# Optimization experiments

Measured on AMD Instinct MI355X. Metric: run time of the kernel, lower is better.

Reference implementation:

```python
import jax, jax.numpy as jnp
import numpy as np

DIM = 768
D_STATE = 16
D_CONV = 4
EXPAND = 2
VOCAB = 50257
N_LAYERS = 4
D_INNER = EXPAND * DIM
B, S = 1, 1024
EPS = 1e-6


def setup_inputs() -> dict:
    key = jax.random.key(0)
    ks = jax.random.split(key, 8)
    s = 0.02
    L = N_LAYERS
    tokens = jax.random.randint(ks[0], (B, S), 0, VOCAB, dtype=jnp.int32)
    embedding = jax.random.normal(ks[1], (VOCAB, DIM), dtype=jnp.float32) * s
    norm_w = jnp.ones((L, DIM), dtype=jnp.float32)
    in_proj_w = jax.random.normal(ks[2], (L, 2 * D_INNER, DIM), dtype=jnp.float32) * s
    conv_w = jax.random.normal(ks[3], (L, D_INNER, 1, D_CONV), dtype=jnp.float32) * s
    conv_b = jnp.zeros((L, D_INNER), dtype=jnp.float32)
    x_proj_w = jax.random.normal(ks[4], (L, D_INNER + 2 * D_STATE, D_INNER), dtype=jnp.float32) * s
    dt_w = jax.random.normal(ks[5], (L, D_INNER, D_INNER), dtype=jnp.float32) * s
    dt_b = jnp.zeros((L, D_INNER), dtype=jnp.float32)
    A_log = jnp.broadcast_to(jnp.log(jnp.arange(1, D_STATE + 1, dtype=jnp.float32)), (L, D_INNER, D_STATE)) + jnp.zeros((L, D_INNER, D_STATE), dtype=jnp.float32)
    D = jnp.ones((L, D_INNER), dtype=jnp.float32)
    out_proj_w = jax.random.normal(ks[6], (L, DIM, D_INNER), dtype=jnp.float32) * s
    normf_w = jnp.ones((DIM,), dtype=jnp.float32)
    lm_head_w = jax.random.normal(ks[7], (VOCAB, DIM), dtype=jnp.float32) * s
    return {"tokens": tokens, "embedding": embedding, "norm_w": norm_w,
            "in_proj_w": in_proj_w, "conv_w": conv_w, "conv_b": conv_b,
            "x_proj_w": x_proj_w, "dt_w": dt_w, "dt_b": dt_b,
            "A_log": A_log, "D": D, "out_proj_w": out_proj_w,
            "normf_w": normf_w, "lm_head_w": lm_head_w}


def _rmsnorm(x, w):
    v = jnp.mean(jnp.square(x.astype(jnp.float32)), axis=-1, keepdims=True)
    return w * (x * jax.lax.rsqrt(v + EPS)).astype(w.dtype)


def _ssm(x, x_proj_w, dt_w, dt_b, A_log, D):
    # x: [B,S,Di]
    xp = jnp.einsum('bsd,ed->bse', x, x_proj_w)  # [B,S,Di+2N]
    dt_in = xp[..., :D_INNER]
    Bm = xp[..., D_INNER:D_INNER + D_STATE]      # [B,S,N]
    Cm = xp[..., D_INNER + D_STATE:]             # [B,S,N]
    dt = jax.nn.softplus(jnp.einsum('bsd,ed->bse', dt_in, dt_w) + dt_b)  # [B,S,Di]
    A = -jnp.exp(A_log)                          # [Di,N]
    dA = jnp.exp(dt[..., None] * A)              # [B,S,Di,N]
    dBx = (dt * x)[..., None] * Bm[:, :, None, :]  # [B,S,Di,N]

    def step(h, inp):
        dA_t, dBx_t, C_t = inp
        h = h * dA_t + dBx_t                     # [B,Di,N]
        y_t = jnp.einsum('bdn,bn->bd', h, C_t)   # [B,Di]
        return h, y_t

    h0 = jnp.zeros((x.shape[0], D_INNER, D_STATE), dtype=x.dtype)
    _, ys = jax.lax.scan(step, h0, (dA.swapaxes(0, 1), dBx.swapaxes(0, 1), Cm.swapaxes(0, 1)))
    return ys.swapaxes(0, 1) + D * x


def _block(x, p):
    nw, ipw, cw, cb, xpw, dtw, dtb, alog, d, opw = p
    res = x
    x = _rmsnorm(x, nw)
    xz = jnp.einsum('bsd,ed->bse', x, ipw)       # [B,S,2*Di]
    xc, z = jnp.split(xz, 2, axis=-1)
    # causal depthwise conv (pad left by d_conv-1, truncate to seq_len)
    xt = xc.transpose(0, 2, 1)                   # [B,Di,S]
    xt = jax.lax.conv_general_dilated(xt, cw, (1,), [(D_CONV - 1, 0)],
                                      dimension_numbers=('NCH', 'OIH', 'NCH'),
                                      feature_group_count=D_INNER)
    xc = xt.transpose(0, 2, 1) + cb
    xc = jax.nn.silu(xc)
    y = _ssm(xc, xpw, dtw, dtb, alog, d)
    out = jnp.einsum('bsd,ed->bse', y * jax.nn.silu(z), opw)
    return res + out


def reference(tokens, embedding, norm_w, in_proj_w, conv_w, conv_b, x_proj_w,
              dt_w, dt_b, A_log, D, out_proj_w, normf_w, lm_head_w):
    x = embedding[tokens]                        # [B,S,DIM]
    params = (norm_w, in_proj_w, conv_w, conv_b, x_proj_w, dt_w, dt_b, A_log, D, out_proj_w)
    x, _ = jax.lax.scan(lambda c, p: (_block(c, p), None), x, params)
    x = _rmsnorm(x, normf_w)
    return jnp.einsum('bsd,vd->bsv', x, lm_head_w)  # logits [B,S,VOCAB]
```

## Files before the change

kernel.cpp:

```cpp
#include <hip/hip_runtime.h>
#include <cstddef>
#include <cstdint>

#define DIM 768
#define DINNER 1536
#define DSTATE 16
#define NLAYERS 4
#define SEQ 1024
#define XPROJ_N 1568
#define VOCAB 50257
#define NCHUNK 128
#define CHL 8

typedef float f32x4 __attribute__((ext_vector_type(4)));
typedef __bf16 bf16x8 __attribute__((ext_vector_type(8)));
typedef __bf16 bf16x4 __attribute__((ext_vector_type(4)));

typedef __attribute__((address_space(1))) const unsigned int as1_u32;
typedef __attribute__((address_space(3))) unsigned int as3_u32;

__device__ __forceinline__ void gl_lds16(const void* g, void* l) {
  __builtin_amdgcn_global_load_lds((as1_u32*)g, (as3_u32*)l, 16, 0, 0);
}

__device__ __forceinline__ float siluf_(float x) {
  return x / (1.f + __expf(-x));
}
__device__ __forceinline__ float softplusf_(float x) {
  return (x > 20.f) ? x : log1pf(expf(x));
}

__global__ __launch_bounds__(256) void k_cvt(const float* __restrict__ src,
                                             __bf16* __restrict__ dst, int n) {
  int e = (blockIdx.x * 256 + threadIdx.x) << 2;
  if (e >= n) return;
  f32x4 v = *(const f32x4*)(src + e);
  bf16x4 h;
  h.x = (__bf16)v.x; h.y = (__bf16)v.y; h.z = (__bf16)v.z; h.w = (__bf16)v.w;
  *(bf16x4*)(dst + e) = h;
}

__global__ __launch_bounds__(256) void k_embed(const int* __restrict__ tok,
                                               const float* __restrict__ emb,
                                               float* __restrict__ X) {
  int i4 = blockIdx.x * 256 + threadIdx.x;
  int s = i4 / 192;
  int d4 = i4 - s * 192;
  const f32x4* src = (const f32x4*)(emb + (size_t)tok[s] * DIM);
  ((f32x4*)X)[i4] = src[d4];
}

__global__ __launch_bounds__(256) void k_rmsnorm(const float* __restrict__ x,
                                                 const float* __restrict__ w,
                                                 __bf16* __restrict__ o) {
  int s = blockIdx.x;
  const float* xr = x + (size_t)s * DIM;
  __bf16* orow = o + (size_t)s * DIM;
  int t = threadIdx.x;
  float v0 = xr[t], v1 = xr[t + 256], v2 = xr[t + 512];
  float acc = v0 * v0 + v1 * v1 + v2 * v2;
#pragma unroll
  for (int m = 32; m >= 1; m >>= 1) acc += __shfl_down(acc, m, 64);
  __shared__ float sred[4];
  if ((t & 63) == 0) sred[t >> 6] = acc;
  __syncthreads();
  float tot = sred[0] + sred[1] + sred[2] + sred[3];
  float rs = rsqrtf(tot * (1.f / 768.f) + 1e-6f);
  orow[t] = (__bf16)(v0 * rs * w[t]);
  orow[t + 256] = (__bf16)(v1 * rs * w[t + 256]);
  orow[t + 512] = (__bf16)(v2 * rs * w[t + 512]);
}

template <int EPI>
__global__ __launch_bounds__(256)
void k_gemm2(const __bf16* __restrict__ A, int lda,
             const __bf16* __restrict__ Wb, int ldb,
             int N, int K,
             float* __restrict__ aux,
             void* __restrict__ Cv, int ldc,
             int zstride) {
  __shared__ __align__(16) __bf16 As[4][64 * 32];
  __shared__ __align__(16) __bf16 Bs[4][64 * 32];
  const int tid = threadIdx.x;
  const int bm = blockIdx.x * 64;
  const int bn = blockIdx.y * 64;
  const int koff = blockIdx.z * K;
  const int lane = tid & 63;
  const int wv = tid >> 6;
  const int wm = (wv >> 1) * 32;
  const int wn = (wv & 1) * 32;
  const int lr = lane & 15;
  const int kb = lane >> 4;
  const int rdoff = ((kb ^ ((lr >> 1) & 3)) << 3);

  f32x4 acc[2][2];
#pragma unroll
  for (int i = 0; i < 2; ++i)
#pragma unroll
    for (int j = 0; j < 2; ++j) acc[i][j] = (f32x4){0.f, 0.f, 0.f, 0.f};

  const int srow = wv * 16 + (lane >> 2);
  const int scs = (((lane & 3) ^ ((lane >> 3) & 3)) << 3);
  const __bf16* Ap = A + (size_t)(bm + srow) * lda + koff + scs;
  int rn0 = bn + srow;
  if (rn0 > N - 1) rn0 = N - 1;
  const __bf16* Bp = Wb + (size_t)rn0 * ldb + koff + scs;

  auto stageA = [&](int b, int kt) {
    gl_lds16(Ap + (kt << 5), &As[b][wv * 512]);
  };
  auto stageB = [&](int b, int kt) {
    gl_lds16(Bp + (kt << 5), &Bs[b][wv * 512]);
  };

  stageA(0, 0); stageB(0, 0);
  stageA(1, 1); stageB(1, 1);
  __syncthreads();

  const int nK = K >> 5;
  int cur = 0;
  for (int kt = 0; kt < nK; kt += 2) {
    const bool more = (kt + 2 < nK);
    if (more) {
      stageA(cur ^ 2, kt + 2); stageB(cur ^ 2, kt + 2);
      stageA((cur ^ 2) | 1, kt + 3); stageB((cur ^ 2) | 1, kt + 3);
    }
#pragma unroll
    for (int s = 0; s < 2; ++s) {
      const int b = cur + s;
      bf16x8 af[2], bfr[2];
#pragma unroll
      for (int i = 0; i < 2; ++i)
        af[i] = *(const bf16x8*)(&As[b][(wm + i * 16 + lr) * 32 + rdoff]);
#pragma unroll
      for (int j = 0; j < 2; ++j)
        bfr[j] = *(const bf16x8*)(&Bs[b][(wn + j * 16 + lr) * 32 + rdoff]);
#pragma unroll
      for (int i = 0; i < 2; ++i)
#pragma unroll
        for (int j = 0; j < 2; ++j)
          acc[i][j] = __builtin_amdgcn_mfma_f32_16x16x32_bf16(bfr[j], af[i], acc[i][j], 0, 0, 0);
    }
    __syncthreads();
    cur ^= 2;
  }

#pragma unroll
  for (int i = 0; i < 2; ++i) {
    const int row = bm + wm + i * 16 + lr;
#pragma unroll
    for (int j = 0; j < 2; ++j) {
      const int col = bn + wn + j * 16 + (kb << 2);
      f32x4 v = acc[i][j];
      if (EPI == 0) {
        if (col < N) {
          bf16x4 h;
          h.x = (__bf16)v.x; h.y = (__bf16)v.y; h.z = (__bf16)v.z; h.w = (__bf16)v.w;
          *(bf16x4*)((__bf16*)Cv + (size_t)row * ldc + col) = h;
        }
      } else if (EPI == 2) {
        if (col < N) {
          float* cp = (float*)Cv + (size_t)row * ldc + col;
          unsafeAtomicAdd(cp + 0, v.x);
          unsafeAtomicAdd(cp + 1, v.y);
          unsafeAtomicAdd(cp + 2, v.z);
          unsafeAtomicAdd(cp + 3, v.w);
        }
      } else if (EPI == 3) {
        float* cp = (float*)Cv + (size_t)blockIdx.z * zstride +
                    (size_t)row * ldc + col;
        if (col + 3 < N) {
          *(f32x4*)cp = v;
        } else {
#pragma unroll
          for (int r = 0; r < 4; ++r)
            if (col + r < N) cp[r] = v[r];
        }
      } else {
        if (col < N) {
          bf16x4 h;
          h.x = (__bf16)v.x; h.y = (__bf16)v.y; h.z = (__bf16)v.z; h.w = (__bf16)v.w;
          *(bf16x4*)((__bf16*)Cv + (size_t)row * ldc + col) = h;
          if (col >= DINNER)
            *(f32x4*)(aux + (size_t)row * 32 + (col - DINNER)) = v;
        }
      }
    }
  }
}

template <int EPI, int SWZ, int TM, int TN>
__global__ __launch_bounds__(256)
void k_gemm(const __bf16* __restrict__ A, int lda,
            const float* __restrict__ Wf, int ldb,
            int N, int K,
            float* __restrict__ aux,
            void* __restrict__ Cv, int ldc,
            int zstride) {
  constexpr int MI = TM / 32;
  constexpr int NJ = TN / 32;
  constexpr int APASS = TM / 64;
  constexpr int BPASS = TN / 32;
  __shared__ __align__(16) __bf16 As[2][TM * 32];
  __shared__ __align__(16) __bf16 Bs[2][TN * 32];
  const int tid = threadIdx.x;
  int bx = blockIdx.x, by = blockIdx.y;
  if (SWZ) {
    const int gx = gridDim.x;
    const int id = by * gx + bx;
    const int cpx = (gx * gridDim.y) >> 3;
    const int id2 = (id & 7) * cpx + (id >> 3);
    bx = id2 % gx;
    by = id2 / gx;
  }
  const int bm = bx * TM;
  const int bn = by * TN;
  const int koff = blockIdx.z * K;
  const int lane = tid & 63;
  const int wv = tid >> 6;
  const int wm = (wv >> 1) * (MI * 16);
  const int wn = (wv & 1) * (TN / 2);
  const int lr = lane & 15;
  const int kb = lane >> 4;
  const int rdoff = ((kb ^ ((lr >> 1) & 3)) << 3);

  f32x4 acc[MI][NJ];
#pragma unroll
  for (int i = 0; i < MI; ++i)
#pragma unroll
    for (int j = 0; j < NJ; ++j) acc[i][j] = (f32x4){0.f, 0.f, 0.f, 0.f};

  const int srow = wv * 16 + (lane >> 2);
  const int scs = (((lane & 3) ^ ((lane >> 3) & 3)) << 3);
  const __bf16* Ap = A + (size_t)(bm + srow) * lda + koff + scs;
  const size_t a64 = (size_t)64 * lda;

  const int r0 = tid >> 3;
  const int c4 = (tid & 7) << 2;
  const int bwr = (((c4 >> 3) ^ ((r0 >> 1) & 3)) << 3) | (c4 & 7);
  const float* Wp = Wf + koff + c4;

  auto stageA = [&](int b, int kt) {
    const int k0 = kt << 5;
#pragma unroll
    for (int ap = 0; ap < APASS; ++ap)
      gl_lds16(Ap + k0 + ap * a64, &As[b][wv * 512 + ap * 2048]);
  };
  f32x4 breg[BPASS];
  auto loadB = [&](int kt) {
#pragma unroll
    for (int p = 0; p < BPASS; ++p) {
      int rn = bn + r0 + (p << 5);
      if (rn > N - 1) rn = N - 1;
      breg[p] = *(const f32x4*)(Wp + (size_t)rn * ldb + (kt << 5));
    }
  };
  auto writeB = [&](int b) {
#pragma unroll
    for (int p = 0; p < BPASS; ++p) {
      bf16x4 bh;
      bh.x = (__bf16)breg[p].x; bh.y = (__bf16)breg[p].y;
      bh.z = (__bf16)breg[p].z; bh.w = (__bf16)breg[p].w;
      *(bf16x4*)(&Bs[b][(r0 + (p << 5)) * 32 + bwr]) = bh;
    }
  };

  stageA(0, 0);
  loadB(0);
  writeB(0);
  __syncthreads();

  const int nK = K >> 5;
  int cur = 0;
  for (int kt = 0; kt < nK; ++kt) {
    const bool more = (kt + 1 < nK);
    if (more) {
      stageA(cur ^ 1, kt + 1);
      loadB(kt + 1);
    }
    bf16x8 af[MI], bfr[NJ];
#pragma unroll
    for (int i = 0; i < MI; ++i)
      af[i] = *(const bf16x8*)(&As[cur][(wm + i * 16 + lr) * 32 + rdoff]);
#pragma unroll
    for (int j = 0; j < NJ; ++j)
      bfr[j] = *(const bf16x8*)(&Bs[cur][(wn + j * 16 + lr) * 32 + rdoff]);
#pragma unroll
    for (int i = 0; i < MI; ++i)
#pragma unroll
      for (int j = 0; j < NJ; ++j)
        acc[i][j] = __builtin_amdgcn_mfma_f32_16x16x32_bf16(bfr[j], af[i], acc[i][j], 0, 0, 0);
    if (more) writeB(cur ^ 1);
    __syncthreads();
    cur ^= 1;
  }

#pragma unroll
  for (int i = 0; i < MI; ++i) {
    const int row = bm + wm + i * 16 + lr;
#pragma unroll
    for (int j = 0; j < NJ; ++j) {
      const int col = bn + wn + j * 16 + (kb << 2);
      f32x4 v = acc[i][j];
      if (EPI == 0) {
        if (col < N) {
          bf16x4 h;
          h.x = (__bf16)v.x; h.y = (__bf16)v.y; h.z = (__bf16)v.z; h.w = (__bf16)v.w;
          *(bf16x4*)((__bf16*)Cv + (size_t)row * ldc + col) = h;
        }
      } else if (EPI == 2) {
        if (col < N) {
          float* cp = (float*)Cv + (size_t)row * ldc + col;
          unsafeAtomicAdd(cp + 0, v.x);
          unsafeAtomicAdd(cp + 1, v.y);
          unsafeAtomicAdd(cp + 2, v.z);
          unsafeAtomicAdd(cp + 3, v.w);
        }
      } else if (EPI == 3) {
        float* cp = (float*)Cv + (size_t)blockIdx.z * zstride +
                    (size_t)row * ldc + col;
        if (col + 3 < N) {
          *(f32x4*)cp = v;
        } else {
#pragma unroll
          for (int r = 0; r < 4; ++r)
            if (col + r < N) cp[r] = v[r];
        }
      } else {
        if (col < N) {
          bf16x4 h;
          h.x = (__bf16)v.x; h.y = (__bf16)v.y; h.z = (__bf16)v.z; h.w = (__bf16)v.w;
          *(bf16x4*)((__bf16*)Cv + (size_t)row * ldc + col) = h;
          if (col >= DINNER)
            *(f32x4*)(aux + (size_t)row * 32 + (col - DINNER)) = v;
        }
      }
    }
  }
}

__global__ __launch_bounds__(384) void k_conv_silu(const __bf16* __restrict__ XZ,
                                                   const float* __restrict__ cw,
                                                   const float* __restrict__ cb,
                                                   __bf16* __restrict__ out) {
  const int s = blockIdx.x;
  const int d = threadIdx.x << 2;
  f32x4 w0 = *(const f32x4*)(cw + (d + 0) * 4);
  f32x4 w1 = *(const f32x4*)(cw + (d + 1) * 4);
  f32x4 w2 = *(const f32x4*)(cw + (d + 2) * 4);
  f32x4 w3 = *(const f32x4*)(cw + (d + 3) * 4);
  f32x4 acc = *(const f32x4*)(cb + d);
#pragma unroll
  for (int k = 0; k < 4; ++k) {
    const int ss = s - 3 + k;
    if (ss >= 0) {
      bf16x4 x = *(const bf16x4*)(XZ + (size_t)ss * (2 * DINNER) + d);
      acc.x += (float)x.x * w0[k];
      acc.y += (float)x.y * w1[k];
      acc.z += (float)x.z * w2[k];
      acc.w += (float)x.w * w3[k];
    }
  }
  bf16x4 o;
  o.x = (__bf16)siluf_(acc.x);
  o.y = (__bf16)siluf_(acc.y);
  o.z = (__bf16)siluf_(acc.z);
  o.w = (__bf16)siluf_(acc.w);
  *(bf16x4*)(out + (size_t)s * DINNER + d) = o;
}

__global__ __launch_bounds__(256) void k_scan1(const float* __restrict__ DT,
                                               const float* __restrict__ dt_b,
                                               const __bf16* __restrict__ XCS,
                                               const float* __restrict__ BC,
                                               const float* __restrict__ A_log,
                                               float* __restrict__ Hloc,
                                               float* __restrict__ Ssum) {
  const int d = blockIdx.x * 256 + threadIdx.x;
  const int c = blockIdx.y;
  const int t0 = c * CHL;
  __shared__ float s_b[CHL][16];
  if (threadIdx.x < CHL * 16) {
    int li = threadIdx.x;
    s_b[li >> 4][li & 15] = BC[(size_t)(t0 + (li >> 4)) * 32 + (li & 15)];
  }
  float a[16];
  const f32x4* alp = (const f32x4*)(A_log + (size_t)d * 16);
#pragma unroll
  for (int q = 0; q < 4; ++q) {
    f32x4 v = alp[q];
    a[q * 4 + 0] = -expf(v.x); a[q * 4 + 1] = -expf(v.y);
    a[q * 4 + 2] = -expf(v.z); a[q * 4 + 3] = -expf(v.w);
  }
  const float bias = dt_b[d];
  float h[16];
#pragma unroll
  for (int n = 0; n < 16; ++n) h[n] = 0.f;
  float ss = 0.f;
  __syncthreads();
#pragma unroll
  for (int tt = 0; tt < CHL; ++tt) {
    const size_t idx = (size_t)(t0 + tt) * DINNER + d;
    const float dtv = softplusf_(DT[idx] + DT[idx + (size_t)SEQ * DINNER] + bias);
    const float xv = (float)XCS[idx];
    const float u = dtv * xv;
    ss += dtv;
#pragma unroll
    for (int n = 0; n < 16; ++n)
      h[n] = h[n] * __expf(dtv * a[n]) + u * s_b[tt][n];
  }
  float* hp = Hloc + ((size_t)c * DINNER + d) * 16;
#pragma unroll
  for (int q = 0; q < 4; ++q)
    ((f32x4*)hp)[q] = (f32x4){h[q * 4], h[q * 4 + 1], h[q * 4 + 2], h[q * 4 + 3]};
  Ssum[(size_t)c * DINNER + d] = ss;
}

__global__ __launch_bounds__(256) void k_scan2(float* __restrict__ H,
                                               const float* __restrict__ Ssum,
                                               const float* __restrict__ A_log) {
  const int idx = blockIdx.x * 256 + threadIdx.x;
  const int d = idx >> 4;
  const float a = -expf(A_log[idx]);
  float h = 0.f;
#pragma unroll 8
  for (int c = 0; c < NCHUNK; ++c) {
    float* p = H + (size_t)c * (DINNER * DSTATE) + idx;
    const float bl = *p;
    const float sv = Ssum[(size_t)c * DINNER + d];
    *p = h;
    h = h * __expf(a * sv) + bl;
  }
}

__global__ __launch_bounds__(256) void k_scan3(const float* __restrict__ DT,
                                               const float* __restrict__ dt_b,
                                               const __bf16* __restrict__ XCS,
                                               const __bf16* __restrict__ XZ,
                                               const float* __restrict__ BC,
                                               const float* __restrict__ A_log,
                                               const float* __restrict__ Dp,
                                               const float* __restrict__ H,
                                               __bf16* __restrict__ Y) {
  const int d = blockIdx.x * 256 + threadIdx.x;
  const int c = blockIdx.y;
  const int t0 = c * CHL;
  __shared__ float s_bc[CHL][32];
  {
    int li = threadIdx.x;
    s_bc[li >> 5][li & 31] = BC[(size_t)(t0 + (li >> 5)) * 32 + (li & 31)];
  }
  float a[16], h[16];
  const f32x4* alp = (const f32x4*)(A_log + (size_t)d * 16);
  const f32x4* hp = (const f32x4*)(H + ((size_t)c * DINNER + d) * 16);
#pragma unroll
  for (int q = 0; q < 4; ++q) {
    f32x4 v = alp[q];
    a[q * 4 + 0] = -expf(v.x); a[q * 4 + 1] = -expf(v.y);
    a[q * 4 + 2] = -expf(v.z); a[q * 4 + 3] = -expf(v.w);
    f32x4 hv = hp[q];
    h[q * 4 + 0] = hv.x; h[q * 4 + 1] = hv.y;
    h[q * 4 + 2] = hv.z; h[q * 4 + 3] = hv.w;
  }
  const float Dd = Dp[d];
  const float bias = dt_b[d];
  __syncthreads();
#pragma unroll
  for (int tt = 0; tt < CHL; ++tt) {
    const size_t idx = (size_t)(t0 + tt) * DINNER + d;
    const float dtv = softplusf_(DT[idx] + DT[idx + (size_t)SEQ * DINNER] + bias);
    const float xv = (float)XCS[idx];
    const float zv = (float)XZ[(size_t)(t0 + tt) * (2 * DINNER) + DINNER + d];
    const float u = dtv * xv;
    float y = 0.f;
#pragma unroll
    for (int n = 0; n < 16; ++n) {
      h[n] = h[n] * __expf(dtv * a[n]) + u * s_bc[tt][n];
      y += h[n] * s_bc[tt][16 + n];
    }
    Y[idx] = (__bf16)((y + Dd * xv) * siluf_(zv));
  }
}

extern "C" void kernel_launch(void* const* d_in, const int* in_sizes, int n_in,
                              void* d_out, int out_size, void* d_ws, size_t ws_size,
                              hipStream_t stream) {
  const int* tokens = (const int*)d_in[0];
  const float* embedding = (const float*)d_in[1];
  const float* norm_w = (const float*)d_in[2];
  const float* in_proj_w = (const float*)d_in[3];
  const float* conv_w = (const float*)d_in[4];
  const float* conv_b = (const float*)d_in[5];
  const float* x_proj_w = (const float*)d_in[6];
  const float* dt_w = (const float*)d_in[7];
  const float* dt_b = (const float*)d_in[8];
  const float* A_log = (const float*)d_in[9];
  const float* Dp = (const float*)d_in[10];
  const float* out_proj_w = (const float*)d_in[11];
  const float* normf_w = (const float*)d_in[12];
  const float* lm_head_w = (const float*)d_in[13];
  float* logits = (float*)d_out;

  char* ws = (char*)d_ws;
  float* X = (float*)(ws + 0);
  __bf16* XN = (__bf16*)(ws + 3145728);
  __bf16* XZ = (__bf16*)(ws + 4718592);
  __bf16* XCS = (__bf16*)(ws + 11010048);
  __bf16* XP = (__bf16*)(ws + 14155776);
  float* DT = (float*)(ws + 17367040);
  float* BC = (float*)(ws + 29949952);
  __bf16* Y = (__bf16*)(ws + 30081024);
  float* Hloc = (float*)(ws + 33226752);
  float* Ssum = (float*)(ws + 45809664);
  __bf16* Wip = (__bf16*)(ws + 46596096);
  __bf16* Wxp = (__bf16*)(ws + 65470464);
  __bf16* Wdt = (__bf16*)(ws + 84738048);
  __bf16* Wop = (__bf16*)(ws + 103612416);
  const bool full = ws_size >= 113049600ull;

  k_embed<<<768, 256, 0, stream>>>(tokens, embedding, X);
  if (full) {
    k_cvt<<<(NLAYERS * 3072 * DIM / 4 + 255) / 256, 256, 0, stream>>>(
        in_proj_w, Wip, NLAYERS * 3072 * DIM);
    k_cvt<<<(NLAYERS * XPROJ_N * DINNER / 4 + 255) / 256, 256, 0, stream>>>(
        x_proj_w, Wxp, NLAYERS * XPROJ_N * DINNER);
    k_cvt<<<(NLAYERS * DINNER * DINNER / 4 + 255) / 256, 256, 0, stream>>>(
        dt_w, Wdt, NLAYERS * DINNER * DINNER);
    k_cvt<<<(NLAYERS * DIM * DINNER / 4 + 255) / 256, 256, 0, stream>>>(
        out_proj_w, Wop, NLAYERS * DIM * DINNER);
  }

  for (int l = 0; l < NLAYERS; ++l) {
    const float* Al = A_log + (size_t)l * DINNER * DSTATE;
    const float* bl = dt_b + (size_t)l * DINNER;

    k_rmsnorm<<<SEQ, 256, 0, stream>>>(X, norm_w + (size_t)l * DIM, XN);
    if (full) {
      k_gemm2<0><<<dim3(16, 48), 256, 0, stream>>>(
          XN, DIM, Wip + (size_t)l * 3072 * DIM, DIM, 2 * DINNER, DIM,
          nullptr, XZ, 2 * DINNER, 0);
    } else {
      k_gemm<0, 0, 64, 64><<<dim3(16, 48), 256, 0, stream>>>(
          XN, DIM, in_proj_w + (size_t)l * 3072 * DIM, DIM, 2 * DINNER,
          DIM, nullptr, XZ, 2 * DINNER, 0);
    }
    k_conv_silu<<<SEQ, 384, 0, stream>>>(
        XZ, conv_w + (size_t)l * DINNER * 4, conv_b + (size_t)l * DINNER, XCS);
    if (full) {
      k_gemm2<4><<<dim3(16, 25), 256, 0, stream>>>(
          XCS, DINNER, Wxp + (size_t)l * XPROJ_N * DINNER, DINNER,
          XPROJ_N, DINNER, BC, XP, XPROJ_N, 0);
      k_gemm2<3><<<dim3(16, 24, 2), 256, 0, stream>>>(
          XP, XPROJ_N, Wdt + (size_t)l * DINNER * DINNER, DINNER, DINNER,
          DINNER / 2, nullptr, DT, DINNER, SEQ * DINNER);
    } else {
      k_gemm<4, 0, 64, 64><<<dim3(16, 25), 256, 0, stream>>>(
          XCS, DINNER, x_proj_w + (size_t)l * XPROJ_N * DINNER, DINNER,
          XPROJ_N, DINNER, BC, XP, XPROJ_N, 0);
      k_gemm<3, 0, 64, 64><<<dim3(16, 24, 2), 256, 0, stream>>>(
          XP, XPROJ_N, dt_w + (size_t)l * DINNER * DINNER, DINNER,
          DINNER, DINNER / 2, nullptr, DT, DINNER, SEQ * DINNER);
    }
    k_scan1<<<dim3(6, NCHUNK), 256, 0, stream>>>(DT, bl, XCS, BC, Al, Hloc, Ssum);
    k_scan2<<<96, 256, 0, stream>>>(Hloc, Ssum, Al);
    k_scan3<<<dim3(6, NCHUNK), 256, 0, stream>>>(DT, bl, XCS, XZ, BC, Al,
                                                 Dp + (size_t)l * DINNER, Hloc, Y);
    if (full) {
      k_gemm2<2><<<dim3(16, 12, 2), 256, 0, stream>>>(
          Y, DINNER, Wop + (size_t)l * DIM * DINNER, DINNER, DIM,
          DINNER / 2, nullptr, X, DIM, 0);
    } else {
      k_gemm<2, 0, 64, 64><<<dim3(16, 12, 2), 256, 0, stream>>>(
          Y, DINNER, out_proj_w + (size_t)l * DIM * DINNER, DINNER,
          DIM, DINNER / 2, nullptr, X, DIM, 0);
    }
  }
  k_rmsnorm<<<SEQ, 256, 0, stream>>>(X, normf_w, XN);
  k_gemm<3, 1, 128, 128><<<dim3(8, 393), 256, 0, stream>>>(
      XN, DIM, lm_head_w, DIM, VOCAB, DIM, nullptr, logits, VOCAB, 0);
}
```

Baseline: 737.2 us.

## Add dedicated LM-head GEMM with 128x64 tiles and merge weight conversion launches

Replaces the 128x128 generic GEMM for the vocab projection with a specialized kernel that uses 128x64 tiles, four LDS stages processing two K-steps per barrier, and register-staged fp32-to-bf16 conversion of the weights with a swizzled layout. The grid doubles, which should fill the GPU better, and the launch order is remapped. The four weight-conversion launches are also fused into one kernel that picks its segment from offsets. Smaller tiles lower reuse of the activation tile and add more blocks.

```diff
diff --git a/kernel.cpp b/kernel.cpp
--- a/kernel.cpp
+++ b/kernel.cpp
@@ -30,14 +30,20 @@
   return (x > 20.f) ? x : log1pf(expf(x));
 }
 
-__global__ __launch_bounds__(256) void k_cvt(const float* __restrict__ src,
-                                             __bf16* __restrict__ dst, int n) {
+struct Cvt4Args {
+  const float* s[4];
+  __bf16* d[4];
+  int off[5];
+};
+__global__ __launch_bounds__(256) void k_cvt4(Cvt4Args a) {
   int e = (blockIdx.x * 256 + threadIdx.x) << 2;
-  if (e >= n) return;
-  f32x4 v = *(const f32x4*)(src + e);
+  if (e >= a.off[4]) return;
+  int seg = (e >= a.off[1]) + (e >= a.off[2]) + (e >= a.off[3]);
+  int le = e - a.off[seg];
+  f32x4 v = *(const f32x4*)(a.s[seg] + le);
   bf16x4 h;
   h.x = (__bf16)v.x; h.y = (__bf16)v.y; h.z = (__bf16)v.z; h.w = (__bf16)v.w;
-  *(bf16x4*)(dst + e) = h;
+  *(bf16x4*)(a.d[seg] + le) = h;
 }
 
 __global__ __launch_bounds__(256) void k_embed(const int* __restrict__ tok,
@@ -189,6 +195,123 @@
   }
 }
 
+__global__ __launch_bounds__(256)
+void k_gemm3(const __bf16* __restrict__ A, int lda,
+             const float* __restrict__ Wf, int ldb,
+             int N, int K, float* __restrict__ C, int ldc) {
+  __shared__ __align__(16) __bf16 As[4][128 * 32];
+  __shared__ __align__(16) __bf16 Bs[4][64 * 32];
+  const int tid = threadIdx.x;
+  int id = blockIdx.y * 8 + blockIdx.x;
+  id = (id & 7) * gridDim.y + (id >> 3);
+  const int bm = (id % 8) * 128;
+  const int bn = (id / 8) * 64;
+  const int lane = tid & 63;
+  const int wv = tid >> 6;
+  const int wm = (wv >> 1) * 64;
+  const int wn = (wv & 1) * 32;
+  const int lr = lane & 15;
+  const int kb = lane >> 4;
+  const int rdoff = ((kb ^ ((lr >> 1) & 3)) << 3);
+
+  f32x4 acc[4][2];
+#pragma unroll
+  for (int i = 0; i < 4; ++i)
+#pragma unroll
+    for (int j = 0; j < 2; ++j) acc[i][j] = (f32x4){0.f, 0.f, 0.f, 0.f};
+
+  const int srow = wv * 16 + (lane >> 2);
+  const int scs = (((lane & 3) ^ ((lane >> 3) & 3)) << 3);
+  const __bf16* Ap = A + (size_t)(bm + srow) * lda + scs;
+  const size_t a64 = (size_t)64 * lda;
+
+  const int r0 = tid >> 3;
+  const int c4 = (tid & 7) << 2;
+  const int bwr = (((c4 >> 3) ^ ((r0 >> 1) & 3)) << 3) | (c4 & 7);
+  const float* Wp = Wf + c4;
+
+  auto stageA = [&](int b, int kt) {
+    const int k0 = kt << 5;
+    gl_lds16(Ap + k0, &As[b][wv * 512]);
+    gl_lds16(Ap + k0 + a64, &As[b][2048 + wv * 512]);
+  };
+  f32x4 breg[2][2];
+  auto loadB = [&](int kt, int s) {
+#pragma unroll
+    for (int p = 0; p < 2; ++p) {
+      int rn = bn + r0 + (p << 5);
+      if (rn > N - 1) rn = N - 1;
+      breg[s][p] = *(const f32x4*)(Wp + (size_t)rn * ldb + (kt << 5));
+    }
+  };
+  auto writeB = [&](int b, int s) {
+#pragma unroll
+    for (int p = 0; p < 2; ++p) {
+      bf16x4 bh;
+      bh.x = (__bf16)breg[s][p].x; bh.y = (__bf16)breg[s][p].y;
+      bh.z = (__bf16)breg[s][p].z; bh.w = (__bf16)breg[s][p].w;
+      *(bf16x4*)(&Bs[b][(r0 + (p << 5)) * 32 + bwr]) = bh;
+    }
+  };
+
+  stageA(0, 0); stageA(1, 1);
+  loadB(0, 0); writeB(0, 0);
+  loadB(1, 1); writeB(1, 1);
+  __syncthreads();
+
+  const int nK = K >> 5;
+  int cur = 0;
+  for (int kt = 0; kt < nK; kt += 2) {
+    const bool more = (kt + 2 < nK);
+    if (more) {
+      stageA(cur ^ 2, kt + 2);
+      stageA((cur ^ 2) | 1, kt + 3);
+      loadB(kt + 2, 0);
+      loadB(kt + 3, 1);
+    }
+#pragma unroll
+    for (int s = 0; s < 2; ++s) {
+      const int b = cur + s;
+      bf16x8 af[4], bfr[2];
+#pragma unroll
+      for (int i = 0; i < 4; ++i)
+        af[i] = *(const bf16x8*)(&As[b][(wm + i * 16 + lr) * 32 + rdoff]);
+#pragma unroll
+      for (int j = 0; j < 2; ++j)
+        bfr[j] = *(const bf16x8*)(&Bs[b][(wn + j * 16 + lr) * 32 + rdoff]);
+#pragma unroll
+      for (int i = 0; i < 4; ++i)
+#pragma unroll
+        for (int j = 0; j < 2; ++j)
+          acc[i][j] = __builtin_amdgcn_mfma_f32_16x16x32_bf16(bfr[j], af[i], acc[i][j], 0, 0, 0);
+    }
+    if (more) {
+      writeB(cur ^ 2, 0);
+      writeB((cur ^ 2) | 1, 1);
+    }
+    __syncthreads();
+    cur ^= 2;
+  }
+
+#pragma unroll
+  for (int i = 0; i < 4; ++i) {
+    const int row = bm + wm + i * 16 + lr;
+#pragma unroll
+    for (int j = 0; j < 2; ++j) {
+      const int col = bn + wn + j * 16 + (kb << 2);
+      float* cp = C + (size_t)row * ldc + col;
+      f32x4 v = acc[i][j];
+      if (col + 3 < N) {
+        *(f32x4*)cp = v;
+      } else {
+#pragma unroll
+        for (int r = 0; r < 4; ++r)
+          if (col + r < N) cp[r] = v[r];
+      }
+    }
+  }
+}
+
 template <int EPI, int SWZ, int TM, int TN>
 __global__ __launch_bounds__(256)
 void k_gemm(const __bf16* __restrict__ A, int lda,
@@ -520,14 +643,17 @@
 
   k_embed<<<768, 256, 0, stream>>>(tokens, embedding, X);
   if (full) {
-    k_cvt<<<(NLAYERS * 3072 * DIM / 4 + 255) / 256, 256, 0, stream>>>(
-        in_proj_w, Wip, NLAYERS * 3072 * DIM);
-    k_cvt<<<(NLAYERS * XPROJ_N * DINNER / 4 + 255) / 256, 256, 0, stream>>>(
-        x_proj_w, Wxp, NLAYERS * XPROJ_N * DINNER);
-    k_cvt<<<(NLAYERS * DINNER * DINNER / 4 + 255) / 256, 256, 0, stream>>>(
-        dt_w, Wdt, NLAYERS * DINNER * DINNER);
-    k_cvt<<<(NLAYERS * DIM * DINNER / 4 + 255) / 256, 256, 0, stream>>>(
-        out_proj_w, Wop, NLAYERS * DIM * DINNER);
+    Cvt4Args ca;
+    ca.s[0] = in_proj_w;  ca.d[0] = Wip;
+    ca.s[1] = x_proj_w;   ca.d[1] = Wxp;
+    ca.s[2] = dt_w;       ca.d[2] = Wdt;
+    ca.s[3] = out_proj_w; ca.d[3] = Wop;
+    ca.off[0] = 0;
+    ca.off[1] = NLAYERS * 3072 * DIM;
+    ca.off[2] = ca.off[1] + NLAYERS * XPROJ_N * DINNER;
+    ca.off[3] = ca.off[2] + NLAYERS * DINNER * DINNER;
+    ca.off[4] = ca.off[3] + NLAYERS * DIM * DINNER;
+    k_cvt4<<<(33226752 / 4 + 255) / 256, 256, 0, stream>>>(ca);
   }
 
   for (int l = 0; l < NLAYERS; ++l) {
@@ -576,6 +702,6 @@
     }
   }
   k_rmsnorm<<<SEQ, 256, 0, stream>>>(X, normf_w, XN);
-  k_gemm<3, 1, 128, 128><<<dim3(8, 393), 256, 0, stream>>>(
-      XN, DIM, lm_head_w, DIM, VOCAB, DIM, nullptr, logits, VOCAB, 0);
-}
+  k_gemm3<<<dim3(8, 786), 256, 0, stream>>>(XN, DIM, lm_head_w, DIM, VOCAB, DIM,
+                                            logits, VOCAB);
+}
```

New measurement: 745.1 us. No clear change (+1.1%).
